# Performance work log

Hardware: AMD Instinct MI355X
Metric: run time of the kernel (lower is better)

The kernel has to match this reference:

```python
import jax, jax.numpy as jnp
import numpy as np

TOP_K = 2

def setup_inputs() -> dict:
    key = jax.random.key(0)
    ks = jax.random.split(key, 5)
    B, T, C, E, H = 4, 2048, 1024, 16, 4096
    x = jax.random.normal(ks[0], (B, T, C), dtype=jnp.float32)
    w_router = jax.random.normal(ks[1], (C, E), dtype=jnp.float32) / np.sqrt(C)
    w1 = jax.random.normal(ks[2], (E, C, H), dtype=jnp.float32) / np.sqrt(C)
    b1 = jnp.zeros((E, H), dtype=jnp.float32)
    w2 = jax.random.normal(ks[3], (E, H, C), dtype=jnp.float32) / np.sqrt(H)
    b2 = jnp.zeros((E, C), dtype=jnp.float32)
    return {"x": x, "w_router": w_router, "w1": w1, "b1": b1, "w2": w2, "b2": b2}


def reference(x, w_router, w1, b1, w2, b2):
    B, T, C = x.shape
    E = w1.shape[0]
    xf = x.reshape(-1, C)                       # [N, C]
    N = xf.shape[0]

    logits = xf @ w_router                      # [N, E]
    rw, sel = jax.lax.top_k(logits, TOP_K)      # [N, K]
    rw = jax.nn.softmax(rw.astype(jnp.float32), axis=-1).astype(x.dtype)

    # combine weight per (token, expert): sum of routing weights over the
    # k-slots that selected that expert (equivalent to the per-k masked loop)
    comb = jnp.zeros((N, E), dtype=x.dtype)
    comb = comb.at[jnp.arange(N)[:, None], sel].add(rw)  # [N, E]

    # loop over experts via scan: out += comb[:, e:e+1] * FFN_e(xf)
    def step(acc, params):
        w1e, b1e, w2e, b2e, ce = params         # ce: [N]
        h = jax.nn.relu(xf @ w1e + b1e)         # [N, 4C]
        y = h @ w2e + b2e                       # [N, C]
        return acc + ce[:, None] * y, None

    out0 = jnp.zeros_like(xf)
    out, _ = jax.lax.scan(step, out0, (w1, b1, w2, b2, comb.T))
    return out.reshape(B, T, C)
```

## Files before the change

kernel.cpp:

```cpp
#include <hip/hip_runtime.h>
#include <hip/hip_bf16.h>


typedef __attribute__((ext_vector_type(4))) float f32x4;
typedef __attribute__((ext_vector_type(8))) __bf16 bf16x8;
typedef __attribute__((ext_vector_type(8))) unsigned short u16x8;

#define NEXP 16
#define CAP  2048
#define CDIM 1024
#define HDIM 4096
#define BM 128
#define BN 128
#define BK 64
#define KS2 2
#define TILE_E (BM * BK)

__device__ __forceinline__ unsigned short f2bf(float f) {
  return __builtin_bit_cast(unsigned short, (__bf16)f);
}

__device__ __forceinline__ int swz(int row, int b) {
  return row * (BK * 2) + (b ^ (((row >> 1) & 7) << 4));
}

typedef __attribute__((address_space(3))) void  lds_void;
typedef __attribute__((address_space(1))) const void gbl_void;
__device__ __forceinline__ void gload16(const void* g, void* l) {
  __builtin_amdgcn_global_load_lds((gbl_void*)g, (lds_void*)l, 16, 0, 0);
}

__device__ __forceinline__ void xcd_remap(int& bx, int& by, int& bz) {
  const int gx = gridDim.x, gy = gridDim.y;
  const int nwg = gx * gy * gridDim.z;
  int flat = blockIdx.x + gx * (blockIdx.y + gy * blockIdx.z);
  flat = (flat & 7) * (nwg >> 3) + (flat >> 3);
  bx = flat % gx;
  const int t = flat / gx;
  by = t % gy;
  bz = t / gy;
}

__global__ __launch_bounds__(64) void router_kernel(
    const float* __restrict__ x, const float* __restrict__ wr,
    float* __restrict__ pair_w, int* __restrict__ counts,
    int* __restrict__ lists)
{
  const int n = blockIdx.x;
  const int l = threadIdx.x;
  const float* xrow = x + (size_t)n * CDIM;
  double acc[NEXP];
#pragma unroll
  for (int e = 0; e < NEXP; e++) acc[e] = 0.0;
  for (int it = 0; it < CDIM / 64; it++) {
    const int c = l + it * 64;
    const double xv = (double)xrow[c];
    const float* w = wr + c * NEXP;
#pragma unroll
    for (int e = 0; e < NEXP; e++) acc[e] += xv * (double)w[e];
  }
#pragma unroll
  for (int e = 0; e < NEXP; e++) {
    double v = acc[e];
    for (int off = 32; off > 0; off >>= 1) v += __shfl_xor(v, off, 64);
    acc[e] = v;
  }
  if (l == 0) {
    int e0 = 0; double b0 = acc[0];
    for (int e = 1; e < NEXP; e++) if (acc[e] > b0) { b0 = acc[e]; e0 = e; }
    int e1 = -1; double b1v = -1e300;
    for (int e = 0; e < NEXP; e++) {
      if (e == e0) continue;
      if (acc[e] > b1v) { b1v = acc[e]; e1 = e; }
    }
    const double d = exp(b1v - b0);
    pair_w[2 * n]     = (float)(1.0 / (1.0 + d));
    pair_w[2 * n + 1] = (float)(d / (1.0 + d));
    int p0 = atomicAdd(&counts[e0], 1);
    if (p0 < CAP) lists[e0 * CAP + p0] = 2 * n;
    int p1 = atomicAdd(&counts[e1], 1);
    if (p1 < CAP) lists[e1 * CAP + p1] = 2 * n + 1;
  }
}

__global__ __launch_bounds__(256) void cvt_x_kernel(
    const float* __restrict__ x, unsigned short* __restrict__ xb, int n8)
{
  const int i = blockIdx.x * 256 + threadIdx.x;
  if (i >= n8) return;
  float4 a = ((const float4*)x)[2 * i];
  float4 b = ((const float4*)x)[2 * i + 1];
  u16x8 v;
  v[0] = f2bf(a.x); v[1] = f2bf(a.y); v[2] = f2bf(a.z); v[3] = f2bf(a.w);
  v[4] = f2bf(b.x); v[5] = f2bf(b.y); v[6] = f2bf(b.z); v[7] = f2bf(b.w);
  ((u16x8*)xb)[i] = v;
}

__global__ __launch_bounds__(256) void transpose_cvt_kernel(
    const float* __restrict__ src, unsigned short* __restrict__ dst,
    int K, int Nn)
{
  __shared__ __align__(16) unsigned short tile[64][72];
  const size_t eoff = (size_t)blockIdx.z * K * Nn;
  const float* S = src + eoff;
  unsigned short* D = dst + eoff;
  const int n0 = blockIdx.x * 64, k0 = blockIdx.y * 64;
  const int t = threadIdx.x;
  {
    const int nl = (t & 15) * 4, kr = t >> 4;
#pragma unroll
    for (int p = 0; p < 4; p++) {
      const int k = kr + p * 16;
      float4 v = *(const float4*)(S + (size_t)(k0 + k) * Nn + n0 + nl);
      tile[nl + 0][k] = f2bf(v.x);
      tile[nl + 1][k] = f2bf(v.y);
      tile[nl + 2][k] = f2bf(v.z);
      tile[nl + 3][k] = f2bf(v.w);
    }
  }
  __syncthreads();
  {
    const int kq = (t & 7) * 8, nr = t >> 3;
#pragma unroll
    for (int p = 0; p < 2; p++) {
      const int n = nr + p * 32;
      u16x8 v = *(const u16x8*)&tile[n][kq];
      *(u16x8*)(D + (size_t)(n0 + n) * K + k0 + kq) = v;
    }
  }
}

#define MFMA_COMPUTE(Abase, Bbase)                                             \
  _Pragma("unroll")                                                            \
  for (int kk = 0; kk < 2; kk++) {                                             \
    bf16x8 af[4], bfr[4];                                                      \
    const int kb = (kk * 32 + lgrp * 8) * 2;                                   \
    _Pragma("unroll")                                                          \
    for (int i = 0; i < 4; i++)                                                \
      af[i] = *(const bf16x8*)((Abase) + swz(wm + i * 16 + lrow, kb));         \
    _Pragma("unroll")                                                          \
    for (int j = 0; j < 4; j++)                                                \
      bfr[j] = *(const bf16x8*)((Bbase) + swz(wn + j * 16 + lrow, kb));        \
    _Pragma("unroll")                                                          \
    for (int i = 0; i < 4; i++)                                                \
      _Pragma("unroll")                                                        \
      for (int j = 0; j < 4; j++)                                              \
        acc[i][j] = __builtin_amdgcn_mfma_f32_16x16x32_bf16(                   \
            af[i], bfr[j], acc[i][j], 0, 0, 0);                                \
  }

__global__ __launch_bounds__(256) void gemm1_async_kernel(
    const unsigned short* __restrict__ xb, const unsigned short* __restrict__ wb,
    const float* __restrict__ b1, const int* __restrict__ counts,
    const int* __restrict__ lists, unsigned short* __restrict__ Hb)
{
  int bx, by, bz;
  xcd_remap(bx, by, bz);
  const int e = bz;
  int cnt = counts[e]; if (cnt > CAP) cnt = CAP;
  const int m0 = by * BM;
  if (m0 >= cnt) return;
  const int n0 = bx * BN;
  const int* list = lists + e * CAP;
  const unsigned short* W = wb + (size_t)e * CDIM * HDIM;

  __shared__ __align__(16) unsigned short As[2 * TILE_E];
  __shared__ __align__(16) unsigned short Bs[2 * TILE_E];

  const int t = threadIdx.x, wid = t >> 6, lane = t & 63;
  const char* ag[4]; const char* bg[4];
  unsigned short* al[4]; unsigned short* bl[4];
#pragma unroll
  for (int i = 0; i < 4; i++) {
    const int r = wid * 32 + i * 8 + (lane >> 3);
    const int cb = ((lane & 7) ^ ((r >> 1) & 7)) << 4;
    int ai = m0 + r; if (ai > cnt - 1) ai = cnt - 1;
    const int tok = list[ai] >> 1;
    ag[i] = (const char*)(xb + (size_t)tok * CDIM) + cb;
    bg[i] = (const char*)(W + (size_t)(n0 + r) * CDIM) + cb;
    al[i] = As + (wid * 32 + i * 8) * BK;
    bl[i] = Bs + (wid * 32 + i * 8) * BK;
  }

  const int wm = (wid >> 1) * 64, wn = (wid & 1) * 64;
  const int lrow = lane & 15, lgrp = lane >> 4;
  f32x4 acc[4][4] = {};

#pragma unroll
  for (int i = 0; i < 4; i++) {
    gload16(ag[i], al[i]);
    gload16(bg[i], bl[i]);
  }
  const int NT = CDIM / BK;
  for (int tt = 0; tt < NT - 1; ++tt) {
    const int p = tt & 1;
    const int koff = (tt + 1) * (BK * 2);
#pragma unroll
    for (int i = 0; i < 4; i++) {
      gload16(ag[i] + koff, al[i] + (p ^ 1) * TILE_E);
      gload16(bg[i] + koff, bl[i] + (p ^ 1) * TILE_E);
    }
    asm volatile("s_waitcnt vmcnt(8)" ::: "memory");
    asm volatile("s_barrier" ::: "memory");
    const char* Ab = (const char*)As + p * (TILE_E * 2);
    const char* Bb = (const char*)Bs + p * (TILE_E * 2);
    MFMA_COMPUTE(Ab, Bb)
    asm volatile("s_barrier" ::: "memory");
  }
  {
    const int p = (NT - 1) & 1;
    asm volatile("s_waitcnt vmcnt(0)" ::: "memory");
    asm volatile("s_barrier" ::: "memory");
    const char* Ab = (const char*)As + p * (TILE_E * 2);
    const char* Bb = (const char*)Bs + p * (TILE_E * 2);
    MFMA_COMPUTE(Ab, Bb)
  }

  int hrow[4][4]; bool valid[4][4];
#pragma unroll
  for (int i = 0; i < 4; i++)
#pragma unroll
    for (int r = 0; r < 4; r++) {
      const int mi = m0 + wm + i * 16 + lgrp * 4 + r;
      valid[i][r] = (mi < cnt);
      hrow[i][r] = list[valid[i][r] ? mi : (cnt - 1)];
    }
#pragma unroll
  for (int j = 0; j < 4; j++) {
    const int col = n0 + wn + j * 16 + lrow;
    const float bias = b1[e * HDIM + col];
#pragma unroll
    for (int i = 0; i < 4; i++)
#pragma unroll
      for (int r = 0; r < 4; r++)
        if (valid[i][r]) {
          float h = acc[i][j][r] + bias;
          h = h > 0.f ? h : 0.f;
          Hb[(size_t)hrow[i][r] * HDIM + col] = f2bf(h);
        }
  }
}

__global__ __launch_bounds__(256) void gemm2_async_kernel(
    const unsigned short* __restrict__ Hb, const unsigned short* __restrict__ wb,
    const float* __restrict__ b2, const float* __restrict__ pair_w,
    const int* __restrict__ counts, const int* __restrict__ lists,
    float* __restrict__ out)
{
  int bx, by, bz;
  xcd_remap(bx, by, bz);
  const int e = bz / KS2, ks = bz % KS2;
  int cnt = counts[e]; if (cnt > CAP) cnt = CAP;
  const int m0 = by * BM;
  if (m0 >= cnt) return;
  const int n0 = bx * BN;
  const int* list = lists + e * CAP;
  const unsigned short* W = wb + (size_t)e * HDIM * CDIM;
  const int kbeg = ks * (HDIM / KS2);

  __shared__ __align__(16) unsigned short As[2 * TILE_E];
  __shared__ __align__(16) unsigned short Bs[2 * TILE_E];

  const int t = threadIdx.x, wid = t >> 6, lane = t & 63;
  const char* ag[4]; const char* bg[4];
  unsigned short* al[4]; unsigned short* bl[4];
#pragma unroll
  for (int i = 0; i < 4; i++) {
    const int r = wid * 32 + i * 8 + (lane >> 3);
    const int cb = ((lane & 7) ^ ((r >> 1) & 7)) << 4;
    int ai = m0 + r; if (ai > cnt - 1) ai = cnt - 1;
    const int pr = list[ai];
    ag[i] = (const char*)(Hb + (size_t)pr * HDIM + kbeg) + cb;
    bg[i] = (const char*)(W + (size_t)(n0 + r) * HDIM + kbeg) + cb;
    al[i] = As + (wid * 32 + i * 8) * BK;
    bl[i] = Bs + (wid * 32 + i * 8) * BK;
  }

  const int wm = (wid >> 1) * 64, wn = (wid & 1) * 64;
  const int lrow = lane & 15, lgrp = lane >> 4;
  f32x4 acc[4][4] = {};

#pragma unroll
  for (int i = 0; i < 4; i++) {
    gload16(ag[i], al[i]);
    gload16(bg[i], bl[i]);
  }
  const int NT = (HDIM / KS2) / BK;
  for (int tt = 0; tt < NT - 1; ++tt) {
    const int p = tt & 1;
    const int koff = (tt + 1) * (BK * 2);
#pragma unroll
    for (int i = 0; i < 4; i++) {
      gload16(ag[i] + koff, al[i] + (p ^ 1) * TILE_E);
      gload16(bg[i] + koff, bl[i] + (p ^ 1) * TILE_E);
    }
    asm volatile("s_waitcnt vmcnt(8)" ::: "memory");
    asm volatile("s_barrier" ::: "memory");
    const char* Ab = (const char*)As + p * (TILE_E * 2);
    const char* Bb = (const char*)Bs + p * (TILE_E * 2);
    MFMA_COMPUTE(Ab, Bb)
    asm volatile("s_barrier" ::: "memory");
  }
  {
    const int p = (NT - 1) & 1;
    asm volatile("s_waitcnt vmcnt(0)" ::: "memory");
    asm volatile("s_barrier" ::: "memory");
    const char* Ab = (const char*)As + p * (TILE_E * 2);
    const char* Bb = (const char*)Bs + p * (TILE_E * 2);
    MFMA_COMPUTE(Ab, Bb)
  }

  float wgt[4][4]; int tok[4][4]; bool valid[4][4];
#pragma unroll
  for (int i = 0; i < 4; i++)
#pragma unroll
    for (int r = 0; r < 4; r++) {
      const int mi = m0 + wm + i * 16 + lgrp * 4 + r;
      valid[i][r] = (mi < cnt);
      const int p = list[valid[i][r] ? mi : (cnt - 1)];
      wgt[i][r] = pair_w[p];
      tok[i][r] = p >> 1;
    }
#pragma unroll
  for (int j = 0; j < 4; j++) {
    const int col = n0 + wn + j * 16 + lrow;
    const float bias = (ks == 0) ? b2[e * CDIM + col] : 0.f;
#pragma unroll
    for (int i = 0; i < 4; i++)
#pragma unroll
      for (int r = 0; r < 4; r++)
        if (valid[i][r])
          atomicAdd(out + (size_t)tok[i][r] * CDIM + col,
                    wgt[i][r] * (acc[i][j][r] + bias));
  }
}

__global__ __launch_bounds__(256) void gemm1_f32_kernel(
    const float* __restrict__ x, const float* __restrict__ w1,
    const float* __restrict__ b1, const int* __restrict__ counts,
    const int* __restrict__ lists, unsigned short* __restrict__ Hb,
    int e_base, int h_by_pair)
{
  const int e = e_base + blockIdx.z;
  int cnt = counts[e]; if (cnt > CAP) cnt = CAP;
  const int m0 = blockIdx.y * BM;
  if (m0 >= cnt) return;
  const int n0 = blockIdx.x * BN;
  const int* list = lists + e * CAP;
  const float* W = w1 + (size_t)e * CDIM * HDIM;
  __shared__ __align__(16) unsigned short As[TILE_E];
  __shared__ __align__(16) unsigned short Bs[TILE_E];
  const int t = threadIdx.x;
  const int a_row = t >> 1, a_half = t & 1;
  int a_idx = m0 + a_row; if (a_idx > cnt - 1) a_idx = cnt - 1;
  const float* a_src = x + (size_t)(list[a_idx] >> 1) * CDIM + a_half * 32;
  const int b_np = t & 63, b_kg = t >> 6;
  const int wid = t >> 6, lane = t & 63;
  const int wm = (wid >> 1) * 64, wn = (wid & 1) * 64;
  const int lrow = lane & 15, lgrp = lane >> 4;
  f32x4 acc[4][4] = {};
  for (int kt = 0; kt < CDIM; kt += BK) {
    {
      const float* s = a_src + kt;
      u16x8 cv[4];
#pragma unroll
      for (int q = 0; q < 4; q++) {
        float4 v0 = *(const float4*)(s + q * 8);
        float4 v1 = *(const float4*)(s + q * 8 + 4);
        cv[q][0] = f2bf(v0.x); cv[q][1] = f2bf(v0.y);
        cv[q][2] = f2bf(v0.z); cv[q][3] = f2bf(v0.w);
        cv[q][4] = f2bf(v1.x); cv[q][5] = f2bf(v1.y);
        cv[q][6] = f2bf(v1.z); cv[q][7] = f2bf(v1.w);
      }
#pragma unroll
      for (int q = 0; q < 4; q++)
        *(u16x8*)((char*)As + swz(a_row, (a_half * 32 + q * 8) * 2)) = cv[q];
    }
    {
#pragma unroll
      for (int it = 0; it < 2; it++) {
        const int k0 = (b_kg + 4 * it) * 8;
        u16x8 c0, c1;
#pragma unroll
        for (int j = 0; j < 8; j++) {
          float2 v = *(const float2*)(W + (size_t)(kt + k0 + j) * HDIM + n0 + 2 * b_np);
          c0[j] = f2bf(v.x); c1[j] = f2bf(v.y);
        }
        *(u16x8*)((char*)Bs + swz(2 * b_np,     k0 * 2)) = c0;
        *(u16x8*)((char*)Bs + swz(2 * b_np + 1, k0 * 2)) = c1;
      }
    }
    __syncthreads();
    MFMA_COMPUTE((const char*)As, (const char*)Bs)
    __syncthreads();
  }
  int hrow[4][4]; bool valid[4][4];
#pragma unroll
  for (int i = 0; i < 4; i++)
#pragma unroll
    for (int r = 0; r < 4; r++) {
      const int mi = m0 + wm + i * 16 + lgrp * 4 + r;
      valid[i][r] = (mi < cnt);
      const int idx = valid[i][r] ? mi : (cnt - 1);
      hrow[i][r] = h_by_pair ? list[idx] : idx;
    }
#pragma unroll
  for (int j = 0; j < 4; j++) {
    const int col = n0 + wn + j * 16 + lrow;
    const float bias = b1[e * HDIM + col];
#pragma unroll
    for (int i = 0; i < 4; i++)
#pragma unroll
      for (int r = 0; r < 4; r++)
        if (valid[i][r]) {
          float h = acc[i][j][r] + bias;
          h = h > 0.f ? h : 0.f;
          Hb[(size_t)hrow[i][r] * HDIM + col] = f2bf(h);
        }
  }
}

__global__ __launch_bounds__(256) void gemm2_f32_kernel(
    const unsigned short* __restrict__ Hb, const float* __restrict__ w2,
    const float* __restrict__ b2, const float* __restrict__ pair_w,
    const int* __restrict__ counts, const int* __restrict__ lists,
    float* __restrict__ out, int e_base, int h_by_pair)
{
  const int e = e_base + blockIdx.z;
  int cnt = counts[e]; if (cnt > CAP) cnt = CAP;
  const int m0 = blockIdx.y * BM;
  if (m0 >= cnt) return;
  const int n0 = blockIdx.x * BN;
  const int* list = lists + e * CAP;
  const float* W = w2 + (size_t)e * HDIM * CDIM;
  __shared__ __align__(16) unsigned short As[TILE_E];
  __shared__ __align__(16) unsigned short Bs[TILE_E];
  const int t = threadIdx.x;
  const int a_row = t >> 1, a_half = t & 1;
  int a_idx = m0 + a_row; if (a_idx > cnt - 1) a_idx = cnt - 1;
  const unsigned short* a_src =
      Hb + (size_t)(h_by_pair ? list[a_idx] : a_idx) * HDIM + a_half * 32;
  const int b_np = t & 63, b_kg = t >> 6;
  const int wid = t >> 6, lane = t & 63;
  const int wm = (wid >> 1) * 64, wn = (wid & 1) * 64;
  const int lrow = lane & 15, lgrp = lane >> 4;
  f32x4 acc[4][4] = {};
  for (int kt = 0; kt < HDIM; kt += BK) {
    {
      const unsigned short* s = a_src + kt;
#pragma unroll
      for (int q = 0; q < 4; q++) {
        u16x8 v = *(const u16x8*)(s + q * 8);
        *(u16x8*)((char*)As + swz(a_row, (a_half * 32 + q * 8) * 2)) = v;
      }
    }
    {
#pragma unroll
      for (int it = 0; it < 2; it++) {
        const int k0 = (b_kg + 4 * it) * 8;
        u16x8 c0, c1;
#pragma unroll
        for (int j = 0; j < 8; j++) {
          float2 v = *(const float2*)(W + (size_t)(kt + k0 + j) * CDIM + n0 + 2 * b_np);
          c0[j] = f2bf(v.x); c1[j] = f2bf(v.y);
        }
        *(u16x8*)((char*)Bs + swz(2 * b_np,     k0 * 2)) = c0;
        *(u16x8*)((char*)Bs + swz(2 * b_np + 1, k0 * 2)) = c1;
      }
    }
    __syncthreads();
    MFMA_COMPUTE((const char*)As, (const char*)Bs)
    __syncthreads();
  }
  float wgt[4][4]; int tok[4][4]; bool valid[4][4];
#pragma unroll
  for (int i = 0; i < 4; i++)
#pragma unroll
    for (int r = 0; r < 4; r++) {
      const int mi = m0 + wm + i * 16 + lgrp * 4 + r;
      valid[i][r] = (mi < cnt);
      const int idx = valid[i][r] ? mi : (cnt - 1);
      const int p = list[idx];
      wgt[i][r] = pair_w[p];
      tok[i][r] = p >> 1;
    }
#pragma unroll
  for (int j = 0; j < 4; j++) {
    const int col = n0 + wn + j * 16 + lrow;
    const float bias = b2[e * CDIM + col];
#pragma unroll
    for (int i = 0; i < 4; i++)
#pragma unroll
      for (int r = 0; r < 4; r++)
        if (valid[i][r])
          atomicAdd(out + (size_t)tok[i][r] * CDIM + col,
                    wgt[i][r] * (acc[i][j][r] + bias));
  }
}

extern "C" void kernel_launch(void* const* d_in, const int* in_sizes, int n_in,
                              void* d_out, int out_size, void* d_ws, size_t ws_size,
                              hipStream_t stream)
{
  const float* x  = (const float*)d_in[0];
  const float* wr = (const float*)d_in[1];
  const float* w1 = (const float*)d_in[2];
  const float* b1 = (const float*)d_in[3];
  const float* w2 = (const float*)d_in[4];
  const float* b2 = (const float*)d_in[5];
  float* out = (float*)d_out;

  const int N = in_sizes[0] / CDIM;

  char* ws = (char*)d_ws;
  int* counts = (int*)ws;
  int* lists  = (int*)(ws + 256);
  float* pw   = (float*)(ws + 256 + NEXP * CAP * 4);
  size_t off = 256 + (size_t)NEXP * CAP * 4 + (size_t)2 * N * 4;
  off = (off + 255) & ~(size_t)255;
  unsigned short* xb = (unsigned short*)(ws + off);
  const size_t xb_sz = (size_t)N * CDIM * 2;
  unsigned short* Hb = (unsigned short*)(ws + off + xb_sz);
  const size_t Hb_sz = (size_t)2 * N * HDIM * 2;
  unsigned short* wb = (unsigned short*)(ws + off + xb_sz + Hb_sz);
  const size_t wb_sz = (size_t)NEXP * CDIM * HDIM * 2;

  const size_t need_new = off + xb_sz + Hb_sz + wb_sz;
  const size_t need_old = off + Hb_sz;

  hipMemsetAsync(d_ws, 0, 64, stream);
  hipMemsetAsync(d_out, 0, (size_t)out_size * 4, stream);

  router_kernel<<<N, 64, 0, stream>>>(x, wr, pw, counts, lists);

  if (ws_size >= need_new) {
    cvt_x_kernel<<<(N * CDIM / 8 + 255) / 256, 256, 0, stream>>>(
        x, xb, N * CDIM / 8);
    transpose_cvt_kernel<<<dim3(HDIM / 64, CDIM / 64, NEXP), 256, 0, stream>>>(
        w1, wb, CDIM, HDIM);
    gemm1_async_kernel<<<dim3(HDIM / BN, CAP / BM, NEXP), 256, 0, stream>>>(
        xb, wb, b1, counts, lists, Hb);
    transpose_cvt_kernel<<<dim3(CDIM / 64, HDIM / 64, NEXP), 256, 0, stream>>>(
        w2, wb, HDIM, CDIM);
    gemm2_async_kernel<<<dim3(CDIM / BN, CAP / BM, NEXP * KS2), 256, 0, stream>>>(
        Hb, wb, b2, pw, counts, lists, out);
  } else if (ws_size >= need_old) {
    unsigned short* Hb0 = (unsigned short*)(ws + off);
    gemm1_f32_kernel<<<dim3(HDIM / BN, CAP / BM, NEXP), 256, 0, stream>>>(
        x, w1, b1, counts, lists, Hb0, 0, 1);
    gemm2_f32_kernel<<<dim3(CDIM / BN, CAP / BM, NEXP), 256, 0, stream>>>(
        Hb0, w2, b2, pw, counts, lists, out, 0, 1);
  }
}
```

Baseline: 1.078 ms.

## Replace expert GEMMs with 256x256-tile, 8-wave kernels using split-K LDS staging

```diff
diff --git a/kernel.cpp b/kernel.cpp
--- a/kernel.cpp
+++ b/kernel.cpp
@@ -10,18 +10,13 @@
 #define CAP  2048
 #define CDIM 1024
 #define HDIM 4096
-#define BM 128
-#define BN 128
-#define BK 64
 #define KS2 2
-#define TILE_E (BM * BK)
+#define BMG 256
+#define BNG 256
+#define SLOT 8192
 
 __device__ __forceinline__ unsigned short f2bf(float f) {
   return __builtin_bit_cast(unsigned short, (__bf16)f);
-}
-
-__device__ __forceinline__ int swz(int row, int b) {
-  return row * (BK * 2) + (b ^ (((row >> 1) & 7) << 4));
 }
 
 typedef __attribute__((address_space(3))) void  lds_void;
@@ -130,7 +125,201 @@
   }
 }
 
-#define MFMA_COMPUTE(Abase, Bbase)                                             \
+
+#define STAGE(parx, hx, koffb)                                                 \
+  do {                                                                         \
+    unsigned short* Ad = &lds[((parx) * 2 + (hx)) * SLOT + w * 512];           \
+    unsigned short* Bd = &lds[4 * SLOT + ((parx) * 2 + (hx)) * SLOT + w * 512];\
+    gload16(agA0 + (koffb), Ad);                                               \
+    gload16(agA1 + (koffb), Ad + 4096);                                        \
+    gload16(bgB0 + (koffb), Bd);                                               \
+    gload16(bgB1 + (koffb), Bd + 4096);                                        \
+  } while (0)
+
+#define COMPUTE(parx, hx)                                                      \
+  do {                                                                         \
+    const unsigned short* As_ = &lds[((parx) * 2 + (hx)) * SLOT];              \
+    const unsigned short* Bs_ = &lds[4 * SLOT + ((parx) * 2 + (hx)) * SLOT];   \
+    bf16x8 af[8], bfv[4];                                                      \
+    _Pragma("unroll")                                                          \
+    for (int mf = 0; mf < 8; mf++)                                             \
+      af[mf] = *(const bf16x8*)(As_ + (wr * 128 + mf * 16 + lrow) * 32 + lgrp * 8); \
+    _Pragma("unroll")                                                          \
+    for (int nf = 0; nf < 4; nf++)                                             \
+      bfv[nf] = *(const bf16x8*)(Bs_ + (wc * 64 + nf * 16 + lrow) * 32 + lgrp * 8); \
+    __builtin_amdgcn_s_setprio(1);                                             \
+    _Pragma("unroll")                                                          \
+    for (int mf = 0; mf < 8; mf++)                                             \
+      _Pragma("unroll")                                                        \
+      for (int nf = 0; nf < 4; nf++)                                           \
+        acc[mf][nf] = __builtin_amdgcn_mfma_f32_16x16x32_bf16(                 \
+            af[mf], bfv[nf], acc[mf][nf], 0, 0, 0);                            \
+    __builtin_amdgcn_s_setprio(0);                                             \
+  } while (0)
+
+#define VMCNT4 asm volatile("s_waitcnt vmcnt(4)" ::: "memory")
+#define VMCNT0 asm volatile("s_waitcnt vmcnt(0)" ::: "memory")
+#define SBAR   asm volatile("s_barrier" ::: "memory")
+
+__global__ __launch_bounds__(512, 2) void gemm1_8p_kernel(
+    const unsigned short* __restrict__ xb, const unsigned short* __restrict__ wb,
+    const float* __restrict__ b1, const int* __restrict__ counts,
+    const int* __restrict__ lists, unsigned short* __restrict__ Hb)
+{
+  int bx, by, bz;
+  xcd_remap(bx, by, bz);
+  const int e = bz;
+  int cnt = counts[e]; if (cnt > CAP) cnt = CAP;
+  const int m0 = by * BMG;
+  if (m0 >= cnt) return;
+  const int n0 = bx * BNG;
+  const int* list = lists + e * CAP;
+  const unsigned short* W = wb + (size_t)e * CDIM * HDIM;
+
+  __shared__ __align__(16) unsigned short lds[8 * SLOT];
+
+  const int t = threadIdx.x, w = t >> 6, lane = t & 63;
+  const int wr = w >> 2, wc = w & 3;
+  const int lrow = lane & 15, lgrp = lane >> 4;
+
+  const int sr0 = w * 16 + (lane >> 2), sr1 = 128 + w * 16 + (lane >> 2);
+  int ai0 = m0 + sr0; if (ai0 > cnt - 1) ai0 = cnt - 1;
+  int ai1 = m0 + sr1; if (ai1 > cnt - 1) ai1 = cnt - 1;
+  const char* agA0 = (const char*)(xb + (size_t)(list[ai0] >> 1) * CDIM) + (lane & 3) * 16;
+  const char* agA1 = (const char*)(xb + (size_t)(list[ai1] >> 1) * CDIM) + (lane & 3) * 16;
+  const char* bgB0 = (const char*)(W + (size_t)(n0 + sr0) * CDIM) + (lane & 3) * 16;
+  const char* bgB1 = (const char*)(W + (size_t)(n0 + sr1) * CDIM) + (lane & 3) * 16;
+
+  f32x4 acc[8][4] = {};
+
+  const int NT = CDIM / 64;
+  STAGE(0, 0, 0);
+  STAGE(0, 1, 64);
+  for (int tt = 0; tt < NT - 1; ++tt) {
+    const int par = tt & 1;
+    const int kofn = (tt + 1) * 128;
+#pragma unroll
+    for (int h = 0; h < 2; ++h) {
+      VMCNT4; SBAR;
+      STAGE(par ^ 1, h, kofn + h * 64);
+      COMPUTE(par, h);
+    }
+  }
+  {
+    const int par = (NT - 1) & 1;
+    VMCNT4; SBAR; COMPUTE(par, 0);
+    VMCNT0; SBAR; COMPUTE(par, 1);
+  }
+
+  int hrow[8][4]; bool valid[8][4];
+#pragma unroll
+  for (int mf = 0; mf < 8; mf++)
+#pragma unroll
+    for (int rr = 0; rr < 4; rr++) {
+      const int mi = m0 + wr * 128 + mf * 16 + lgrp * 4 + rr;
+      valid[mf][rr] = (mi < cnt);
+      hrow[mf][rr] = list[valid[mf][rr] ? mi : (cnt - 1)];
+    }
+#pragma unroll
+  for (int nf = 0; nf < 4; nf++) {
+    const int col = n0 + wc * 64 + nf * 16 + lrow;
+    const float bias = b1[e * HDIM + col];
+#pragma unroll
+    for (int mf = 0; mf < 8; mf++)
+#pragma unroll
+      for (int rr = 0; rr < 4; rr++)
+        if (valid[mf][rr]) {
+          float h = acc[mf][nf][rr] + bias;
+          h = h > 0.f ? h : 0.f;
+          Hb[(size_t)hrow[mf][rr] * HDIM + col] = f2bf(h);
+        }
+  }
+}
+
+__global__ __launch_bounds__(512, 2) void gemm2_8p_kernel(
+    const unsigned short* __restrict__ Hb, const unsigned short* __restrict__ wb,
+    const float* __restrict__ b2, const float* __restrict__ pair_w,
+    const int* __restrict__ counts, const int* __restrict__ lists,
+    float* __restrict__ out)
+{
+  int bx, by, bz;
+  xcd_remap(bx, by, bz);
+  const int e = bz / KS2, ks = bz % KS2;
+  int cnt = counts[e]; if (cnt > CAP) cnt = CAP;
+  const int m0 = by * BMG;
+  if (m0 >= cnt) return;
+  const int n0 = bx * BNG;
+  const int* list = lists + e * CAP;
+  const unsigned short* W = wb + (size_t)e * HDIM * CDIM;
+  const int kbegb = ks * (HDIM / KS2) * 2;
+
+  __shared__ __align__(16) unsigned short lds[8 * SLOT];
+
+  const int t = threadIdx.x, w = t >> 6, lane = t & 63;
+  const int wr = w >> 2, wc = w & 3;
+  const int lrow = lane & 15, lgrp = lane >> 4;
+
+  const int sr0 = w * 16 + (lane >> 2), sr1 = 128 + w * 16 + (lane >> 2);
+  int ai0 = m0 + sr0; if (ai0 > cnt - 1) ai0 = cnt - 1;
+  int ai1 = m0 + sr1; if (ai1 > cnt - 1) ai1 = cnt - 1;
+  const char* agA0 = (const char*)(Hb + (size_t)list[ai0] * HDIM) + kbegb + (lane & 3) * 16;
+  const char* agA1 = (const char*)(Hb + (size_t)list[ai1] * HDIM) + kbegb + (lane & 3) * 16;
+  const char* bgB0 = (const char*)(W + (size_t)(n0 + sr0) * HDIM) + kbegb + (lane & 3) * 16;
+  const char* bgB1 = (const char*)(W + (size_t)(n0 + sr1) * HDIM) + kbegb + (lane & 3) * 16;
+
+  f32x4 acc[8][4] = {};
+
+  const int NT = (HDIM / KS2) / 64;
+  STAGE(0, 0, 0);
+  STAGE(0, 1, 64);
+  for (int tt = 0; tt < NT - 1; ++tt) {
+    const int par = tt & 1;
+    const int kofn = (tt + 1) * 128;
+#pragma unroll
+    for (int h = 0; h < 2; ++h) {
+      VMCNT4; SBAR;
+      STAGE(par ^ 1, h, kofn + h * 64);
+      COMPUTE(par, h);
+    }
+  }
+  {
+    const int par = (NT - 1) & 1;
+    VMCNT4; SBAR; COMPUTE(par, 0);
+    VMCNT0; SBAR; COMPUTE(par, 1);
+  }
+
+  float wgt[8][4]; int tok[8][4]; bool valid[8][4];
+#pragma unroll
+  for (int mf = 0; mf < 8; mf++)
+#pragma unroll
+    for (int rr = 0; rr < 4; rr++) {
+      const int mi = m0 + wr * 128 + mf * 16 + lgrp * 4 + rr;
+      valid[mf][rr] = (mi < cnt);
+      const int p = list[valid[mf][rr] ? mi : (cnt - 1)];
+      wgt[mf][rr] = pair_w[p];
+      tok[mf][rr] = p >> 1;
+    }
+#pragma unroll
+  for (int nf = 0; nf < 4; nf++) {
+    const int col = n0 + wc * 64 + nf * 16 + lrow;
+    const float bias = (ks == 0) ? b2[e * CDIM + col] : 0.f;
+#pragma unroll
+    for (int mf = 0; mf < 8; mf++)
+#pragma unroll
+      for (int rr = 0; rr < 4; rr++)
+        if (valid[mf][rr])
+          atomicAdd(out + (size_t)tok[mf][rr] * CDIM + col,
+                    wgt[mf][rr] * (acc[mf][nf][rr] + bias));
+  }
+}
+
+typedef __attribute__((ext_vector_type(8))) unsigned short u16x8b;
+
+__device__ __forceinline__ int swz(int row, int b) {
+  return row * 128 + (b ^ (((row >> 1) & 7) << 4));
+}
+
+#define MFMA_COMPUTE_F(Abase, Bbase)                                           \
   _Pragma("unroll")                                                            \
   for (int kk = 0; kk < 2; kk++) {                                             \
     bf16x8 af[4], bfr[4];                                                      \
@@ -149,192 +338,6 @@
             af[i], bfr[j], acc[i][j], 0, 0, 0);                                \
   }
 
-__global__ __launch_bounds__(256) void gemm1_async_kernel(
-    const unsigned short* __restrict__ xb, const unsigned short* __restrict__ wb,
-    const float* __restrict__ b1, const int* __restrict__ counts,
-    const int* __restrict__ lists, unsigned short* __restrict__ Hb)
-{
-  int bx, by, bz;
-  xcd_remap(bx, by, bz);
-  const int e = bz;
-  int cnt = counts[e]; if (cnt > CAP) cnt = CAP;
-  const int m0 = by * BM;
-  if (m0 >= cnt) return;
-  const int n0 = bx * BN;
-  const int* list = lists + e * CAP;
-  const unsigned short* W = wb + (size_t)e * CDIM * HDIM;
-
-  __shared__ __align__(16) unsigned short As[2 * TILE_E];
-  __shared__ __align__(16) unsigned short Bs[2 * TILE_E];
-
-  const int t = threadIdx.x, wid = t >> 6, lane = t & 63;
-  const char* ag[4]; const char* bg[4];
-  unsigned short* al[4]; unsigned short* bl[4];
-#pragma unroll
-  for (int i = 0; i < 4; i++) {
-    const int r = wid * 32 + i * 8 + (lane >> 3);
-    const int cb = ((lane & 7) ^ ((r >> 1) & 7)) << 4;
-    int ai = m0 + r; if (ai > cnt - 1) ai = cnt - 1;
-    const int tok = list[ai] >> 1;
-    ag[i] = (const char*)(xb + (size_t)tok * CDIM) + cb;
-    bg[i] = (const char*)(W + (size_t)(n0 + r) * CDIM) + cb;
-    al[i] = As + (wid * 32 + i * 8) * BK;
-    bl[i] = Bs + (wid * 32 + i * 8) * BK;
-  }
-
-  const int wm = (wid >> 1) * 64, wn = (wid & 1) * 64;
-  const int lrow = lane & 15, lgrp = lane >> 4;
-  f32x4 acc[4][4] = {};
-
-#pragma unroll
-  for (int i = 0; i < 4; i++) {
-    gload16(ag[i], al[i]);
-    gload16(bg[i], bl[i]);
-  }
-  const int NT = CDIM / BK;
-  for (int tt = 0; tt < NT - 1; ++tt) {
-    const int p = tt & 1;
-    const int koff = (tt + 1) * (BK * 2);
-#pragma unroll
-    for (int i = 0; i < 4; i++) {
-      gload16(ag[i] + koff, al[i] + (p ^ 1) * TILE_E);
-      gload16(bg[i] + koff, bl[i] + (p ^ 1) * TILE_E);
-    }
-    asm volatile("s_waitcnt vmcnt(8)" ::: "memory");
-    asm volatile("s_barrier" ::: "memory");
-    const char* Ab = (const char*)As + p * (TILE_E * 2);
-    const char* Bb = (const char*)Bs + p * (TILE_E * 2);
-    MFMA_COMPUTE(Ab, Bb)
-    asm volatile("s_barrier" ::: "memory");
-  }
-  {
-    const int p = (NT - 1) & 1;
-    asm volatile("s_waitcnt vmcnt(0)" ::: "memory");
-    asm volatile("s_barrier" ::: "memory");
-    const char* Ab = (const char*)As + p * (TILE_E * 2);
-    const char* Bb = (const char*)Bs + p * (TILE_E * 2);
-    MFMA_COMPUTE(Ab, Bb)
-  }
-
-  int hrow[4][4]; bool valid[4][4];
-#pragma unroll
-  for (int i = 0; i < 4; i++)
-#pragma unroll
-    for (int r = 0; r < 4; r++) {
-      const int mi = m0 + wm + i * 16 + lgrp * 4 + r;
-      valid[i][r] = (mi < cnt);
-      hrow[i][r] = list[valid[i][r] ? mi : (cnt - 1)];
-    }
-#pragma unroll
-  for (int j = 0; j < 4; j++) {
-    const int col = n0 + wn + j * 16 + lrow;
-    const float bias = b1[e * HDIM + col];
-#pragma unroll
-    for (int i = 0; i < 4; i++)
-#pragma unroll
-      for (int r = 0; r < 4; r++)
-        if (valid[i][r]) {
-          float h = acc[i][j][r] + bias;
-          h = h > 0.f ? h : 0.f;
-          Hb[(size_t)hrow[i][r] * HDIM + col] = f2bf(h);
-        }
-  }
-}
-
-__global__ __launch_bounds__(256) void gemm2_async_kernel(
-    const unsigned short* __restrict__ Hb, const unsigned short* __restrict__ wb,
-    const float* __restrict__ b2, const float* __restrict__ pair_w,
-    const int* __restrict__ counts, const int* __restrict__ lists,
-    float* __restrict__ out)
-{
-  int bx, by, bz;
-  xcd_remap(bx, by, bz);
-  const int e = bz / KS2, ks = bz % KS2;
-  int cnt = counts[e]; if (cnt > CAP) cnt = CAP;
-  const int m0 = by * BM;
-  if (m0 >= cnt) return;
-  const int n0 = bx * BN;
-  const int* list = lists + e * CAP;
-  const unsigned short* W = wb + (size_t)e * HDIM * CDIM;
-  const int kbeg = ks * (HDIM / KS2);
-
-  __shared__ __align__(16) unsigned short As[2 * TILE_E];
-  __shared__ __align__(16) unsigned short Bs[2 * TILE_E];
-
-  const int t = threadIdx.x, wid = t >> 6, lane = t & 63;
-  const char* ag[4]; const char* bg[4];
-  unsigned short* al[4]; unsigned short* bl[4];
-#pragma unroll
-  for (int i = 0; i < 4; i++) {
-    const int r = wid * 32 + i * 8 + (lane >> 3);
-    const int cb = ((lane & 7) ^ ((r >> 1) & 7)) << 4;
-    int ai = m0 + r; if (ai > cnt - 1) ai = cnt - 1;
-    const int pr = list[ai];
-    ag[i] = (const char*)(Hb + (size_t)pr * HDIM + kbeg) + cb;
-    bg[i] = (const char*)(W + (size_t)(n0 + r) * HDIM + kbeg) + cb;
-    al[i] = As + (wid * 32 + i * 8) * BK;
-    bl[i] = Bs + (wid * 32 + i * 8) * BK;
-  }
-
-  const int wm = (wid >> 1) * 64, wn = (wid & 1) * 64;
-  const int lrow = lane & 15, lgrp = lane >> 4;
-  f32x4 acc[4][4] = {};
-
-#pragma unroll
-  for (int i = 0; i < 4; i++) {
-    gload16(ag[i], al[i]);
-    gload16(bg[i], bl[i]);
-  }
-  const int NT = (HDIM / KS2) / BK;
-  for (int tt = 0; tt < NT - 1; ++tt) {
-    const int p = tt & 1;
-    const int koff = (tt + 1) * (BK * 2);
-#pragma unroll
-    for (int i = 0; i < 4; i++) {
-      gload16(ag[i] + koff, al[i] + (p ^ 1) * TILE_E);
-      gload16(bg[i] + koff, bl[i] + (p ^ 1) * TILE_E);
-    }
-    asm volatile("s_waitcnt vmcnt(8)" ::: "memory");
-    asm volatile("s_barrier" ::: "memory");
-    const char* Ab = (const char*)As + p * (TILE_E * 2);
-    const char* Bb = (const char*)Bs + p * (TILE_E * 2);
-    MFMA_COMPUTE(Ab, Bb)
-    asm volatile("s_barrier" ::: "memory");
-  }
-  {
-    const int p = (NT - 1) & 1;
-    asm volatile("s_waitcnt vmcnt(0)" ::: "memory");
-    asm volatile("s_barrier" ::: "memory");
-    const char* Ab = (const char*)As + p * (TILE_E * 2);
-    const char* Bb = (const char*)Bs + p * (TILE_E * 2);
-    MFMA_COMPUTE(Ab, Bb)
-  }
-
-  float wgt[4][4]; int tok[4][4]; bool valid[4][4];
-#pragma unroll
-  for (int i = 0; i < 4; i++)
-#pragma unroll
-    for (int r = 0; r < 4; r++) {
-      const int mi = m0 + wm + i * 16 + lgrp * 4 + r;
-      valid[i][r] = (mi < cnt);
-      const int p = list[valid[i][r] ? mi : (cnt - 1)];
-      wgt[i][r] = pair_w[p];
-      tok[i][r] = p >> 1;
-    }
-#pragma unroll
-  for (int j = 0; j < 4; j++) {
-    const int col = n0 + wn + j * 16 + lrow;
-    const float bias = (ks == 0) ? b2[e * CDIM + col] : 0.f;
-#pragma unroll
-    for (int i = 0; i < 4; i++)
-#pragma unroll
-      for (int r = 0; r < 4; r++)
-        if (valid[i][r])
-          atomicAdd(out + (size_t)tok[i][r] * CDIM + col,
-                    wgt[i][r] * (acc[i][j][r] + bias));
-  }
-}
-
 __global__ __launch_bounds__(256) void gemm1_f32_kernel(
     const float* __restrict__ x, const float* __restrict__ w1,
     const float* __restrict__ b1, const int* __restrict__ counts,
@@ -343,13 +346,13 @@
 {
   const int e = e_base + blockIdx.z;
   int cnt = counts[e]; if (cnt > CAP) cnt = CAP;
-  const int m0 = blockIdx.y * BM;
+  const int m0 = blockIdx.y * 128;
   if (m0 >= cnt) return;
-  const int n0 = blockIdx.x * BN;
+  const int n0 = blockIdx.x * 128;
   const int* list = lists + e * CAP;
   const float* W = w1 + (size_t)e * CDIM * HDIM;
-  __shared__ __align__(16) unsigned short As[TILE_E];
-  __shared__ __align__(16) unsigned short Bs[TILE_E];
+  __shared__ __align__(16) unsigned short As[128 * 64];
+  __shared__ __align__(16) unsigned short Bs[128 * 64];
   const int t = threadIdx.x;
   const int a_row = t >> 1, a_half = t & 1;
   int a_idx = m0 + a_row; if (a_idx > cnt - 1) a_idx = cnt - 1;
@@ -359,7 +362,7 @@
   const int wm = (wid >> 1) * 64, wn = (wid & 1) * 64;
   const int lrow = lane & 15, lgrp = lane >> 4;
   f32x4 acc[4][4] = {};
-  for (int kt = 0; kt < CDIM; kt += BK) {
+  for (int kt = 0; kt < CDIM; kt += 64) {
     {
       const float* s = a_src + kt;
       u16x8 cv[4];
@@ -391,7 +394,7 @@
       }
     }
     __syncthreads();
-    MFMA_COMPUTE((const char*)As, (const char*)Bs)
+    MFMA_COMPUTE_F((const char*)As, (const char*)Bs)
     __syncthreads();
   }
   int hrow[4][4]; bool valid[4][4];
@@ -428,13 +431,13 @@
 {
   const int e = e_base + blockIdx.z;
   int cnt = counts[e]; if (cnt > CAP) cnt = CAP;
-  const int m0 = blockIdx.y * BM;
+  const int m0 = blockIdx.y * 128;
   if (m0 >= cnt) return;
-  const int n0 = blockIdx.x * BN;
+  const int n0 = blockIdx.x * 128;
   const int* list = lists + e * CAP;
   const float* W = w2 + (size_t)e * HDIM * CDIM;
-  __shared__ __align__(16) unsigned short As[TILE_E];
-  __shared__ __align__(16) unsigned short Bs[TILE_E];
+  __shared__ __align__(16) unsigned short As[128 * 64];
+  __shared__ __align__(16) unsigned short Bs[128 * 64];
   const int t = threadIdx.x;
   const int a_row = t >> 1, a_half = t & 1;
   int a_idx = m0 + a_row; if (a_idx > cnt - 1) a_idx = cnt - 1;
@@ -445,7 +448,7 @@
   const int wm = (wid >> 1) * 64, wn = (wid & 1) * 64;
   const int lrow = lane & 15, lgrp = lane >> 4;
   f32x4 acc[4][4] = {};
-  for (int kt = 0; kt < HDIM; kt += BK) {
+  for (int kt = 0; kt < HDIM; kt += 64) {
     {
       const unsigned short* s = a_src + kt;
 #pragma unroll
@@ -469,7 +472,7 @@
       }
     }
     __syncthreads();
-    MFMA_COMPUTE((const char*)As, (const char*)Bs)
+    MFMA_COMPUTE_F((const char*)As, (const char*)Bs)
     __syncthreads();
   }
   float wgt[4][4]; int tok[4][4]; bool valid[4][4];
@@ -538,17 +541,17 @@
         x, xb, N * CDIM / 8);
     transpose_cvt_kernel<<<dim3(HDIM / 64, CDIM / 64, NEXP), 256, 0, stream>>>(
         w1, wb, CDIM, HDIM);
-    gemm1_async_kernel<<<dim3(HDIM / BN, CAP / BM, NEXP), 256, 0, stream>>>(
+    gemm1_8p_kernel<<<dim3(HDIM / BNG, CAP / BMG, NEXP), 512, 0, stream>>>(
         xb, wb, b1, counts, lists, Hb);
     transpose_cvt_kernel<<<dim3(CDIM / 64, HDIM / 64, NEXP), 256, 0, stream>>>(
         w2, wb, HDIM, CDIM);
-    gemm2_async_kernel<<<dim3(CDIM / BN, CAP / BM, NEXP * KS2), 256, 0, stream>>>(
+    gemm2_8p_kernel<<<dim3(CDIM / BNG, CAP / BMG, NEXP * KS2), 512, 0, stream>>>(
         Hb, wb, b2, pw, counts, lists, out);
   } else if (ws_size >= need_old) {
     unsigned short* Hb0 = (unsigned short*)(ws + off);
-    gemm1_f32_kernel<<<dim3(HDIM / BN, CAP / BM, NEXP), 256, 0, stream>>>(
+    gemm1_f32_kernel<<<dim3(HDIM / 128, CAP / 128, NEXP), 256, 0, stream>>>(
         x, w1, b1, counts, lists, Hb0, 0, 1);
-    gemm2_f32_kernel<<<dim3(CDIM / BN, CAP / BM, NEXP), 256, 0, stream>>>(
+    gemm2_f32_kernel<<<dim3(CDIM / 128, CAP / 128, NEXP), 256, 0, stream>>>(
         Hb0, w2, b2, pw, counts, lists, out, 0, 1);
   }
 }
```

After: 937.5 us. 1.15x faster.
